# Optimization experiments

Hardware: AMD Instinct MI355X
Metric: run time of the kernel (lower is better)

The kernel has to match this reference:

```python
import jax, jax.numpy as jnp
import numpy as np

B, S, E = 2, 2048, 1024
H, D = 16, 64
BASE = 10000.0


def rotate_half(x):
    x1, x2 = jnp.split(x, 2, axis=-1)
    return jnp.concatenate((-x2, x1), axis=-1)


def rope_cos_sin(seq_len, dim):
    inv_freq = 1.0 / (BASE ** (jnp.arange(0, dim, 2, dtype=jnp.float32) / dim))
    t = jnp.arange(seq_len, dtype=jnp.float32)
    freqs = jnp.einsum('i,j->ij', t, inv_freq)          # [S, D/2]
    emb = jnp.concatenate((freqs, freqs), axis=-1)       # [S, D]
    return jnp.cos(emb), jnp.sin(emb)


def setup_inputs() -> dict:
    key = jax.random.key(0)
    ks = jax.random.split(key, 9)
    s = 1.0 / np.sqrt(E)
    inp = {
        'x': jax.random.normal(ks[0], (B, S, E), dtype=jnp.float32),
        'mask': jnp.ones((B, S), dtype=jnp.int32),
        'Wq': jax.random.normal(ks[1], (E, H * D), dtype=jnp.float32) * s,
        'bq': jnp.zeros((H * D,), dtype=jnp.float32),
        'Wk': jax.random.normal(ks[2], (E, H * D), dtype=jnp.float32) * s,
        'bk': jnp.zeros((H * D,), dtype=jnp.float32),
        'Wv': jax.random.normal(ks[3], (E, H * D), dtype=jnp.float32) * s,
        'bv': jnp.zeros((H * D,), dtype=jnp.float32),
        'Wo': jax.random.normal(ks[4], (H * D, E), dtype=jnp.float32) * s,
        'bo': jnp.zeros((E,), dtype=jnp.float32),
    }
    return inp


def reference(x, mask, Wq, bq, Wk, bk, Wv, bv, Wo, bo):
    b, s, _ = x.shape
    scale = D ** (-0.5)
    # projections -> [B, H, S, D]
    q = (x @ Wq + bq).reshape(b, s, H, D).transpose(0, 2, 1, 3)
    k = (x @ Wk + bk).reshape(b, s, H, D).transpose(0, 2, 1, 3)
    v = (x @ Wv + bv).reshape(b, s, H, D).transpose(0, 2, 1, 3)
    # rotary position embedding
    cos, sin = rope_cos_sin(s, D)                      # [S, D]
    cos = cos[None, None]
    sin = sin[None, None]
    q = q * cos + rotate_half(q) * sin
    k = k * cos + rotate_half(k) * sin
    # scores [B, H, S, S]
    scores = jnp.einsum('bhqd,bhkd->bhqk', q, k) * scale
    # padding mask [B,1,1,S]
    scores = jnp.where(mask[:, None, None, :] == 0, -jnp.inf, scores)
    # causal mask
    i = jnp.arange(s)
    causal = jnp.where(i[None, :] > i[:, None], -jnp.inf, 0.0)  # [S, S]
    scores = scores + causal[None, None]
    attn = jax.nn.softmax(scores, axis=-1)
    ctx = jnp.einsum('bhqk,bhkd->bhqd', attn, v)
    ctx = ctx.transpose(0, 2, 1, 3).reshape(b, s, H * D)
    return ctx @ Wo + bo
```

## Files before the change

kernel.cpp:

```cpp
#include <hip/hip_runtime.h>
#include <cstdint>
#include <cstddef>

#define DEVI __device__ __forceinline__

typedef __bf16 bf16_t;
typedef __bf16 bf16x4 __attribute__((ext_vector_type(4)));
typedef __bf16 bf16x8 __attribute__((ext_vector_type(8)));
typedef float  f32x4  __attribute__((ext_vector_type(4)));
typedef unsigned short u16x4 __attribute__((ext_vector_type(4)));

static constexpr int Bz = 2, S = 2048, E = 1024, H = 16, Dh = 64;
static constexpr int M  = Bz * S;
static constexpr int N  = H * Dh;
static constexpr int Kd = E;

DEVI unsigned short f2bf(float f) {
  unsigned u = __builtin_bit_cast(unsigned, f);
  return (unsigned short)((u + 0x7fffu + ((u >> 16) & 1u)) >> 16);
}

DEVI void async_copy16(void* lds, const void* g) {
  __builtin_amdgcn_global_load_lds((__attribute__((address_space(1))) void*)(g),
                                   (__attribute__((address_space(3))) void*)(lds), 16, 0, 0);
}

__global__ void prep_kernel(const float* __restrict__ x, bf16_t* __restrict__ xb,
                            const float* __restrict__ Wq, const float* __restrict__ Wk,
                            const float* __restrict__ Wv, const float* __restrict__ Wo,
                            bf16_t* __restrict__ WtBase,
                            float* __restrict__ ropeC, float* __restrict__ ropeS) {
  __shared__ unsigned short tile[64][68];
  const int blk = blockIdx.x, tid = threadIdx.x;
  if (blk < 4096) {
    int i = blk * 256 + tid;
    float4 v = ((const float4*)x)[i];
    u16x4 o = { f2bf(v.x), f2bf(v.y), f2bf(v.z), f2bf(v.w) };
    ((u16x4*)xb)[i] = o;
  } else if (blk < 5120) {
    const int i = blk - 4096;
    const int z = i >> 8, rest = i & 255;
    const int n0 = (rest & 15) * 64, k0 = (rest >> 4) * 64;
    const float* W = (z == 0) ? Wq : (z == 1) ? Wk : (z == 2) ? Wv : Wo;
    unsigned short* T = (unsigned short*)(WtBase + (size_t)z * Kd * N);
    for (int e = tid; e < 1024; e += 256) {
      int r = e >> 4, c4 = (e & 15) * 4;
      float4 v = *(const float4*)(W + (size_t)(k0 + r) * N + n0 + c4);
      u16x4 o = { f2bf(v.x), f2bf(v.y), f2bf(v.z), f2bf(v.w) };
      *(u16x4*)&tile[r][c4] = o;
    }
    __syncthreads();
    for (int e = tid; e < 1024; e += 256) {
      int r = e >> 4, c4 = (e & 15) * 4;
      u16x4 o = { tile[c4][r], tile[c4 + 1][r], tile[c4 + 2][r], tile[c4 + 3][r] };
      *(u16x4*)&T[(size_t)(n0 + r) * Kd + k0 + c4] = o;
    }
  } else {
    int i = (blk - 5120) * 256 + tid;
    int pos = i >> 5, j = i & 31;
    float inv = exp2f(-(float)j * 0.41524101186092029f);
    float ang = (float)pos * inv;
    ropeC[i] = cosf(ang);
    ropeS[i] = sinf(ang);
  }
}

__global__ void vtrans_kernel(const bf16_t* __restrict__ V, bf16_t* __restrict__ Vt) {
  __shared__ unsigned short tile[64][68];
  const int bh = blockIdx.y;
  const int s0 = blockIdx.x * 64;
  const unsigned short* Vp = (const unsigned short*)V + (size_t)bh * S * Dh;
  unsigned short* Tp = (unsigned short*)Vt + (size_t)bh * Dh * S;
  const int tid = threadIdx.x;
  for (int e = tid; e < 1024; e += 256) {
    int r = e >> 4, c4 = (e & 15) * 4;
    u16x4 v = *(const u16x4*)(Vp + (size_t)(s0 + r) * Dh + c4);
    *(u16x4*)&tile[r][c4] = v;
  }
  __syncthreads();
  for (int e = tid; e < 1024; e += 256) {
    int d = e >> 4, s4 = (e & 15) * 4;
    u16x4 o = { tile[s4][d], tile[s4 + 1][d], tile[s4 + 2][d], tile[s4 + 3][d] };
    *(u16x4*)&Tp[(size_t)d * S + s0 + s4] = o;
  }
}


DEVI void gemm_mainloop(const bf16_t* __restrict__ A, const bf16_t* __restrict__ Bt,
                        bf16_t* sA, bf16_t* sB, int m0, int n0, f32x4 (&acc)[4][4]) {
  const int tid  = threadIdx.x;
  const int lane = tid & 63;
  const int wid  = tid >> 6;
  const int l16  = lane & 15;
  const int quad = lane >> 4;
  const int wm = (wid >> 1) * 64;
  const int wn = (wid & 1) * 64;
  const int o0 = wid * 2048 + lane * 16;
  const int o1 = o0 + 1024;
  const int r0 = o0 >> 6, c0 = o0 & 63;
  const int r1 = o1 >> 6, c1 = o1 & 63;
  const char* Ab = (const char*)A;
  const char* Bb = (const char*)Bt;
  char* sAc = (char*)sA;
  char* sBc = (char*)sB;

  for (int k0 = 0; k0 < Kd; k0 += 32) {
    __syncthreads();
    async_copy16(sAc + wid * 2048,        Ab + ((size_t)(m0 + r0) * Kd + k0) * 2 + c0);
    async_copy16(sAc + wid * 2048 + 1024, Ab + ((size_t)(m0 + r1) * Kd + k0) * 2 + c1);
    async_copy16(sBc + wid * 2048,        Bb + ((size_t)(n0 + r0) * Kd + k0) * 2 + c0);
    async_copy16(sBc + wid * 2048 + 1024, Bb + ((size_t)(n0 + r1) * Kd + k0) * 2 + c1);
    __syncthreads();
    bf16x8 af[4], bfv[4];
#pragma unroll
    for (int mi = 0; mi < 4; ++mi)
      af[mi] = *(const bf16x8*)(sA + (wm + mi * 16 + l16) * 32 + quad * 8);
#pragma unroll
    for (int ni = 0; ni < 4; ++ni)
      bfv[ni] = *(const bf16x8*)(sB + (wn + ni * 16 + l16) * 32 + quad * 8);
#pragma unroll
    for (int mi = 0; mi < 4; ++mi)
#pragma unroll
      for (int ni = 0; ni < 4; ++ni)
        acc[mi][ni] = __builtin_amdgcn_mfma_f32_16x16x32_bf16(af[mi], bfv[ni], acc[mi][ni], 0, 0, 0);
  }
}

__global__ __launch_bounds__(256, 3) void gemm_qkv_kernel(
    const bf16_t* __restrict__ xb, const bf16_t* __restrict__ WtBase,
    const float* __restrict__ bq, const float* __restrict__ bk, const float* __restrict__ bv,
    bf16_t* __restrict__ outBase,
    const float* __restrict__ ropeC, const float* __restrict__ ropeS) {
  __shared__ bf16_t sA[4096], sB[4096];
  const int z = blockIdx.z;
  const bf16_t* Bt = WtBase + (size_t)z * Kd * N;
  const float* bias = (z == 0) ? bq : (z == 1) ? bk : bv;
  unsigned short* outp = (unsigned short*)(outBase + (size_t)z * M * N);
  const int n0 = blockIdx.x * 128, m0 = blockIdx.y * 128;
  f32x4 acc[4][4] = {};
  gemm_mainloop(xb, Bt, sA, sB, m0, n0, acc);

  const int tid = threadIdx.x, lane = tid & 63, wid = tid >> 6;
  const int l16 = lane & 15, quad = lane >> 4;
  const int wm = (wid >> 1) * 64, wn = (wid & 1) * 64;
  const int cbase = n0 + wn;
  const int h = cbase >> 6;

  if (z < 2) {
    const float qs = (z == 0) ? 0.18033688011112042f : 1.0f;
#pragma unroll
    for (int mi = 0; mi < 4; ++mi)
#pragma unroll
      for (int r = 0; r < 4; ++r) {
        int t = m0 + wm + mi * 16 + quad * 4 + r;
        int bb = t >> 11, s = t & (S - 1);
        size_t obase = ((size_t)(bb * H + h) * S + s) * Dh;
#pragma unroll
        for (int np = 0; np < 2; ++np) {
          int j = np * 16 + l16;
          float cc = ropeC[s * 32 + j];
          float ss = ropeS[s * 32 + j];
          float xlo = acc[mi][np][r]     + bias[cbase + j];
          float xhi = acc[mi][np + 2][r] + bias[cbase + j + 32];
          outp[obase + j]      = f2bf((xlo * cc - xhi * ss) * qs);
          outp[obase + j + 32] = f2bf((xhi * cc + xlo * ss) * qs);
        }
      }
  } else {
#pragma unroll
    for (int mi = 0; mi < 4; ++mi)
#pragma unroll
      for (int r = 0; r < 4; ++r) {
        int t = m0 + wm + mi * 16 + quad * 4 + r;
        int bb = t >> 11, s = t & (S - 1);
        size_t obase = ((size_t)(bb * H + h) * S + s) * Dh;
#pragma unroll
        for (int ni = 0; ni < 4; ++ni) {
          int d = ni * 16 + l16;
          outp[obase + d] = f2bf(acc[mi][ni][r] + bias[cbase + d]);
        }
      }
  }
}

__global__ __launch_bounds__(256, 4) void gemm_o_kernel(
    const bf16_t* __restrict__ A, const bf16_t* __restrict__ Bt,
    const float* __restrict__ bias, float* __restrict__ out) {
  __shared__ bf16_t sA[2048], sB[4096];
  const int n0 = blockIdx.x * 128, m0 = blockIdx.y * 64;
  const int tid = threadIdx.x, lane = tid & 63, wid = tid >> 6;
  const int l16 = lane & 15, quad = lane >> 4;
  const int wm = (wid >> 1) * 32, wn = (wid & 1) * 64;
  const int rowoff = lane >> 2, col8 = (lane & 3) * 8;
  const char* Ab = (const char*)A;
  const char* Bb = (const char*)Bt;
  char* sAc = (char*)sA;
  char* sBc = (char*)sB;
  f32x4 acc[2][4] = {};

  for (int k0 = 0; k0 < Kd; k0 += 32) {
    __syncthreads();
    async_copy16(sAc + wid * 1024,
                 Ab + ((size_t)(m0 + wid * 16 + rowoff) * Kd + k0 + col8) * 2);
    async_copy16(sBc + (wid * 2) * 1024,
                 Bb + ((size_t)(n0 + wid * 32 + rowoff) * Kd + k0 + col8) * 2);
    async_copy16(sBc + (wid * 2 + 1) * 1024,
                 Bb + ((size_t)(n0 + wid * 32 + 16 + rowoff) * Kd + k0 + col8) * 2);
    __syncthreads();
    bf16x8 af[2], bfv[4];
#pragma unroll
    for (int mi = 0; mi < 2; ++mi)
      af[mi] = *(const bf16x8*)(sA + (wm + mi * 16 + l16) * 32 + quad * 8);
#pragma unroll
    for (int ni = 0; ni < 4; ++ni)
      bfv[ni] = *(const bf16x8*)(sB + (wn + ni * 16 + l16) * 32 + quad * 8);
#pragma unroll
    for (int mi = 0; mi < 2; ++mi)
#pragma unroll
      for (int ni = 0; ni < 4; ++ni)
        acc[mi][ni] = __builtin_amdgcn_mfma_f32_16x16x32_bf16(af[mi], bfv[ni], acc[mi][ni], 0, 0, 0);
  }
#pragma unroll
  for (int mi = 0; mi < 2; ++mi)
#pragma unroll
    for (int r = 0; r < 4; ++r) {
      int t = m0 + wm + mi * 16 + quad * 4 + r;
#pragma unroll
      for (int ni = 0; ni < 4; ++ni) {
        int c = n0 + wn + ni * 16 + l16;
        out[(size_t)t * N + c] = acc[mi][ni][r] + bias[c];
      }
    }
}

__global__ __launch_bounds__(256, 3) void attn_kernel(
    const bf16_t* __restrict__ Q, const bf16_t* __restrict__ Kb,
    const bf16_t* __restrict__ Vt, const int* __restrict__ mask,
    bf16_t* __restrict__ ctx) {
  __shared__ bf16_t sK[8192];
  __shared__ bf16_t sV[8192];
  __shared__ unsigned short sP[4][16 * 136];

  const int tid = threadIdx.x, lane = tid & 63, wid = tid >> 6;
  const int l16 = lane & 15, quad = lane >> 4;

  const int idx = blockIdx.x;
  const int qb  = 31 - (idx >> 5);
  const int bh  = idx & 31;
  const int b   = bh >> 4;
  const int q0  = qb * 64;
  const int qw  = q0 + wid * 16;

  const bf16_t* Qp = Q + ((size_t)bh * S + qw) * Dh;
  const char*   Kg = (const char*)(Kb + (size_t)bh * S * Dh);
  const char*   Vg = (const char*)(Vt + (size_t)bh * Dh * S);
  const int*    mp = mask + b * S;

  bf16x8 qf0 = *(const bf16x8*)(Qp + l16 * Dh + quad * 8);
  bf16x8 qf1 = *(const bf16x8*)(Qp + l16 * Dh + 32 + quad * 8);

  int    sLds[4];
  size_t kGo[4], vGo[4];
#pragma unroll
  for (int i = 0; i < 4; ++i) {
    int sk = wid * 4 + i;
    int g = sk >> 1, c = sk & 1;
    sLds[i] = sk * 1024;
    kGo[i] = ((size_t)(g * 16 + l16) * Dh + c * 32 + quad * 8) * 2;
    vGo[i] = ((size_t)(wid * 16 + l16) * S + i * 32 + quad * 8) * 2;
  }
  char* sKc = (char*)sK;
  char* sVc = (char*)sV;

  f32x4 acc[4] = {};
  float lsum = 0.f;
  const int qcol = qw + l16;
  const int niter = (qb >> 1) + 1;
  unsigned short* pb = &sP[wid][0];

  for (int kt = 0; kt < niter; ++kt) {
    const int kb = kt * 128;
    __syncthreads();
#pragma unroll
    for (int i = 0; i < 4; ++i) {
      async_copy16(sKc + sLds[i], Kg + (size_t)kb * (Dh * 2) + kGo[i]);
      async_copy16(sVc + sLds[i], Vg + (size_t)kb * 2 + vGo[i]);
    }
    int mk0 = mp[kb + lane];
    int mk1 = mp[kb + 64 + lane];
    __syncthreads();

    f32x4 st[8];
#pragma unroll
    for (int g = 0; g < 8; ++g) {
      bf16x8 kf0 = *(const bf16x8*)(sK + (g * 2 + 0) * 512 + lane * 8);
      bf16x8 kf1 = *(const bf16x8*)(sK + (g * 2 + 1) * 512 + lane * 8);
      f32x4 z = {};
      z = __builtin_amdgcn_mfma_f32_16x16x32_bf16(kf0, qf0, z, 0, 0, 0);
      z = __builtin_amdgcn_mfma_f32_16x16x32_bf16(kf1, qf1, z, 0, 0, 0);
      st[g] = z;
    }

    unsigned long long dm0 = __ballot(mk0 == 0);
    unsigned long long dm1 = __ballot(mk1 == 0);
    if (dm0 | dm1) {
#pragma unroll
      for (int g = 0; g < 8; ++g) {
        unsigned long long dm = (g < 4) ? dm0 : dm1;
#pragma unroll
        for (int r = 0; r < 4; ++r)
          if ((dm >> ((g & 3) * 16 + quad * 4 + r)) & 1ull) st[g][r] = -1e30f;
      }
    }
    if (kt == niter - 1) {
#pragma unroll
      for (int g = 0; g < 8; ++g)
#pragma unroll
        for (int r = 0; r < 4; ++r)
          if (kb + g * 16 + quad * 4 + r > qcol) st[g][r] = -1e30f;
    }

#pragma unroll
    for (int g = 0; g < 8; ++g) {
      float e0 = exp2f(st[g][0]), e1 = exp2f(st[g][1]);
      float e2 = exp2f(st[g][2]), e3 = exp2f(st[g][3]);
      lsum += (e0 + e1) + (e2 + e3);
      bf16x4 pk = { (bf16_t)e0, (bf16_t)e1, (bf16_t)e2, (bf16_t)e3 };
      *(bf16x4*)&pb[l16 * 136 + g * 16 + quad * 4] = pk;
    }
    bf16x8 pf[4];
#pragma unroll
    for (int kc = 0; kc < 4; ++kc)
      pf[kc] = *(const bf16x8*)((const bf16_t*)(const void*)pb + l16 * 136 + kc * 32 + quad * 8);

#pragma unroll
    for (int dt = 0; dt < 4; ++dt)
#pragma unroll
      for (int kc = 0; kc < 4; ++kc) {
        bf16x8 vf = *(const bf16x8*)(sV + (dt * 4 + kc) * 512 + lane * 8);
        acc[dt] = __builtin_amdgcn_mfma_f32_16x16x32_bf16(vf, pf[kc], acc[dt], 0, 0, 0);
      }
  }

  lsum += __shfl_xor(lsum, 16);
  lsum += __shfl_xor(lsum, 32);
  float inv = 1.0f / lsum;
  unsigned short* cp = (unsigned short*)ctx;
  size_t trow = ((size_t)(b * S + qw + l16)) * N + (size_t)(bh & 15) * Dh;
#pragma unroll
  for (int dt = 0; dt < 4; ++dt) {
    u16x4 o = { f2bf(acc[dt][0] * inv), f2bf(acc[dt][1] * inv),
                f2bf(acc[dt][2] * inv), f2bf(acc[dt][3] * inv) };
    *(u16x4*)&cp[trow + dt * 16 + quad * 4] = o;
  }
}


extern "C" void kernel_launch(void* const* d_in, const int* in_sizes, int n_in,
                              void* d_out, int out_size, void* d_ws, size_t ws_size,
                              hipStream_t stream) {
  const float* x  = (const float*)d_in[0];
  const int*  msk = (const int*)d_in[1];
  const float* Wq = (const float*)d_in[2];
  const float* bq = (const float*)d_in[3];
  const float* Wk = (const float*)d_in[4];
  const float* bk = (const float*)d_in[5];
  const float* Wv = (const float*)d_in[6];
  const float* bv = (const float*)d_in[7];
  const float* Wo = (const float*)d_in[8];
  const float* bo = (const float*)d_in[9];
  float* out = (float*)d_out;
  (void)in_sizes; (void)n_in; (void)out_size; (void)ws_size;

  char* ws = (char*)d_ws;
  bf16_t* xb   = (bf16_t*)(ws);
  bf16_t* WT   = (bf16_t*)(ws + (8u  << 20));
  bf16_t* qkv  = (bf16_t*)(ws + (16u << 20));
  bf16_t* Qb   = qkv;
  bf16_t* Kbuf = qkv + (size_t)1 * M * N;
  bf16_t* Vb   = qkv + (size_t)2 * M * N;
  bf16_t* Vt   = xb;
  bf16_t* ctx  = Vb;
  float* ropeC = (float*)(ws + (40u << 20));
  float* ropeS = ropeC + (size_t)S * 32;

  prep_kernel<<<5376, 256, 0, stream>>>(x, xb, Wq, Wk, Wv, Wo, WT, ropeC, ropeS);
  gemm_qkv_kernel<<<dim3(8, 32, 3), 256, 0, stream>>>(xb, WT, bq, bk, bv, qkv, ropeC, ropeS);
  vtrans_kernel<<<dim3(32, 32), 256, 0, stream>>>(Vb, Vt);
  attn_kernel<<<1024, 256, 0, stream>>>(Qb, Kbuf, Vt, msk, ctx);
  gemm_o_kernel<<<dim3(8, 64), 256, 0, stream>>>(ctx, WT + (size_t)3 * Kd * N, bo, out);
}
```

Baseline: 197.9 us.

## Double-buffer GEMM and attention tiles; switch attention to 32x32 MFMA with 128-row query blocks

Both GEMM mainloops and the attention kernel now double-buffer their LDS tiles, issuing the async global-to-LDS copy for the next K step before computing on the current one, and drop one barrier per iteration. The attention kernel is restructured so each wave handles 32 query rows with 32x32x16 bf16 MFMAs over 64-key tiles, in 128-row query blocks with half as many workgroups. Waves skip key tiles that lie fully beyond their causal limit. The aim is to hide load latency and raise MFMA efficiency, at the cost of more LDS per block, possible occupancy loss and a new output-normalisation path through LDS.

```diff
diff --git a/kernel.cpp b/kernel.cpp
--- a/kernel.cpp
+++ b/kernel.cpp
@@ -8,6 +8,7 @@
 typedef __bf16 bf16x4 __attribute__((ext_vector_type(4)));
 typedef __bf16 bf16x8 __attribute__((ext_vector_type(8)));
 typedef float  f32x4  __attribute__((ext_vector_type(4)));
+typedef float  f32x16 __attribute__((ext_vector_type(16)));
 typedef unsigned short u16x4 __attribute__((ext_vector_type(4)));
 
 static constexpr int Bz = 2, S = 2048, E = 1024, H = 16, Dh = 64;
@@ -104,20 +105,26 @@
   char* sAc = (char*)sA;
   char* sBc = (char*)sB;
 
-  for (int k0 = 0; k0 < Kd; k0 += 32) {
+  auto stage = [&](int buf, int k0) {
+    async_copy16(sAc + buf * 8192 + wid * 2048,        Ab + ((size_t)(m0 + r0) * Kd + k0) * 2 + c0);
+    async_copy16(sAc + buf * 8192 + wid * 2048 + 1024, Ab + ((size_t)(m0 + r1) * Kd + k0) * 2 + c1);
+    async_copy16(sBc + buf * 8192 + wid * 2048,        Bb + ((size_t)(n0 + r0) * Kd + k0) * 2 + c0);
+    async_copy16(sBc + buf * 8192 + wid * 2048 + 1024, Bb + ((size_t)(n0 + r1) * Kd + k0) * 2 + c1);
+  };
+
+  stage(0, 0);
+  for (int i = 0; i < Kd / 32; ++i) {
     __syncthreads();
-    async_copy16(sAc + wid * 2048,        Ab + ((size_t)(m0 + r0) * Kd + k0) * 2 + c0);
-    async_copy16(sAc + wid * 2048 + 1024, Ab + ((size_t)(m0 + r1) * Kd + k0) * 2 + c1);
-    async_copy16(sBc + wid * 2048,        Bb + ((size_t)(n0 + r0) * Kd + k0) * 2 + c0);
-    async_copy16(sBc + wid * 2048 + 1024, Bb + ((size_t)(n0 + r1) * Kd + k0) * 2 + c1);
-    __syncthreads();
+    if (i + 1 < Kd / 32) stage((i + 1) & 1, (i + 1) * 32);
+    const bf16_t* a = sA + (i & 1) * 4096;
+    const bf16_t* b = sB + (i & 1) * 4096;
     bf16x8 af[4], bfv[4];
 #pragma unroll
     for (int mi = 0; mi < 4; ++mi)
-      af[mi] = *(const bf16x8*)(sA + (wm + mi * 16 + l16) * 32 + quad * 8);
+      af[mi] = *(const bf16x8*)(a + (wm + mi * 16 + l16) * 32 + quad * 8);
 #pragma unroll
     for (int ni = 0; ni < 4; ++ni)
-      bfv[ni] = *(const bf16x8*)(sB + (wn + ni * 16 + l16) * 32 + quad * 8);
+      bfv[ni] = *(const bf16x8*)(b + (wn + ni * 16 + l16) * 32 + quad * 8);
 #pragma unroll
     for (int mi = 0; mi < 4; ++mi)
 #pragma unroll
@@ -131,14 +138,14 @@
     const float* __restrict__ bq, const float* __restrict__ bk, const float* __restrict__ bv,
     bf16_t* __restrict__ outBase,
     const float* __restrict__ ropeC, const float* __restrict__ ropeS) {
-  __shared__ bf16_t sA[4096], sB[4096];
+  __shared__ bf16_t sA[2][4096], sB[2][4096];
   const int z = blockIdx.z;
   const bf16_t* Bt = WtBase + (size_t)z * Kd * N;
   const float* bias = (z == 0) ? bq : (z == 1) ? bk : bv;
   unsigned short* outp = (unsigned short*)(outBase + (size_t)z * M * N);
   const int n0 = blockIdx.x * 128, m0 = blockIdx.y * 128;
   f32x4 acc[4][4] = {};
-  gemm_mainloop(xb, Bt, sA, sB, m0, n0, acc);
+  gemm_mainloop(xb, Bt, &sA[0][0], &sB[0][0], m0, n0, acc);
 
   const int tid = threadIdx.x, lane = tid & 63, wid = tid >> 6;
   const int l16 = lane & 15, quad = lane >> 4;
@@ -186,7 +193,7 @@
 __global__ __launch_bounds__(256, 4) void gemm_o_kernel(
     const bf16_t* __restrict__ A, const bf16_t* __restrict__ Bt,
     const float* __restrict__ bias, float* __restrict__ out) {
-  __shared__ bf16_t sA[2048], sB[4096];
+  __shared__ bf16_t sA[2][2048], sB[2][4096];
   const int n0 = blockIdx.x * 128, m0 = blockIdx.y * 64;
   const int tid = threadIdx.x, lane = tid & 63, wid = tid >> 6;
   const int l16 = lane & 15, quad = lane >> 4;
@@ -198,22 +205,28 @@
   char* sBc = (char*)sB;
   f32x4 acc[2][4] = {};
 
-  for (int k0 = 0; k0 < Kd; k0 += 32) {
+  auto stage = [&](int buf, int k0) {
+    async_copy16(sAc + buf * 4096 + wid * 1024,
+                 Ab + ((size_t)(m0 + wid * 16 + rowoff) * Kd + k0 + col8) * 2);
+    async_copy16(sBc + buf * 8192 + (wid * 2) * 1024,
+                 Bb + ((size_t)(n0 + wid * 32 + rowoff) * Kd + k0 + col8) * 2);
+    async_copy16(sBc + buf * 8192 + (wid * 2 + 1) * 1024,
+                 Bb + ((size_t)(n0 + wid * 32 + 16 + rowoff) * Kd + k0 + col8) * 2);
+  };
+
+  stage(0, 0);
+  for (int i = 0; i < Kd / 32; ++i) {
     __syncthreads();
-    async_copy16(sAc + wid * 1024,
-                 Ab + ((size_t)(m0 + wid * 16 + rowoff) * Kd + k0 + col8) * 2);
-    async_copy16(sBc + (wid * 2) * 1024,
-                 Bb + ((size_t)(n0 + wid * 32 + rowoff) * Kd + k0 + col8) * 2);
-    async_copy16(sBc + (wid * 2 + 1) * 1024,
-                 Bb + ((size_t)(n0 + wid * 32 + 16 + rowoff) * Kd + k0 + col8) * 2);
-    __syncthreads();
+    if (i + 1 < Kd / 32) stage((i + 1) & 1, (i + 1) * 32);
+    const bf16_t* a = &sA[0][0] + (i & 1) * 2048;
+    const bf16_t* b = &sB[0][0] + (i & 1) * 4096;
     bf16x8 af[2], bfv[4];
 #pragma unroll
     for (int mi = 0; mi < 2; ++mi)
-      af[mi] = *(const bf16x8*)(sA + (wm + mi * 16 + l16) * 32 + quad * 8);
+      af[mi] = *(const bf16x8*)(a + (wm + mi * 16 + l16) * 32 + quad * 8);
 #pragma unroll
     for (int ni = 0; ni < 4; ++ni)
-      bfv[ni] = *(const bf16x8*)(sB + (wn + ni * 16 + l16) * 32 + quad * 8);
+      bfv[ni] = *(const bf16x8*)(b + (wn + ni * 16 + l16) * 32 + quad * 8);
 #pragma unroll
     for (int mi = 0; mi < 2; ++mi)
 #pragma unroll
@@ -237,122 +250,138 @@
     const bf16_t* __restrict__ Q, const bf16_t* __restrict__ Kb,
     const bf16_t* __restrict__ Vt, const int* __restrict__ mask,
     bf16_t* __restrict__ ctx) {
-  __shared__ bf16_t sK[8192];
-  __shared__ bf16_t sV[8192];
-  __shared__ unsigned short sP[4][16 * 136];
+  __shared__ bf16_t sK[2][4096];
+  __shared__ bf16_t sV[2][4096];
+  __shared__ unsigned short sP[4][32 * 72];
 
   const int tid = threadIdx.x, lane = tid & 63, wid = tid >> 6;
-  const int l16 = lane & 15, quad = lane >> 4;
-
-  const int idx = blockIdx.x;
-  const int qb  = 31 - (idx >> 5);
-  const int bh  = idx & 31;
-  const int b   = bh >> 4;
-  const int q0  = qb * 64;
-  const int qw  = q0 + wid * 16;
+  const int l32 = lane & 31, half = lane >> 5;
+
+  const int idx  = blockIdx.x;
+  const int qblk = 15 - (idx >> 5);
+  const int bh   = idx & 31;
+  const int b    = bh >> 4;
+  const int q0   = qblk * 128;
+  const int qw   = q0 + wid * 32;
 
   const bf16_t* Qp = Q + ((size_t)bh * S + qw) * Dh;
   const char*   Kg = (const char*)(Kb + (size_t)bh * S * Dh);
   const char*   Vg = (const char*)(Vt + (size_t)bh * Dh * S);
   const int*    mp = mask + b * S;
 
-  bf16x8 qf0 = *(const bf16x8*)(Qp + l16 * Dh + quad * 8);
-  bf16x8 qf1 = *(const bf16x8*)(Qp + l16 * Dh + 32 + quad * 8);
-
-  int    sLds[4];
-  size_t kGo[4], vGo[4];
-#pragma unroll
-  for (int i = 0; i < 4; ++i) {
-    int sk = wid * 4 + i;
-    int g = sk >> 1, c = sk & 1;
-    sLds[i] = sk * 1024;
-    kGo[i] = ((size_t)(g * 16 + l16) * Dh + c * 32 + quad * 8) * 2;
-    vGo[i] = ((size_t)(wid * 16 + l16) * S + i * 32 + quad * 8) * 2;
-  }
+  bf16x8 qf[4];
+#pragma unroll
+  for (int c = 0; c < 4; ++c)
+    qf[c] = *(const bf16x8*)(Qp + l32 * Dh + c * 16 + half * 8);
+
+  const int ks0 = wid * 2, ks1 = wid * 2 + 1;
+  const size_t kOff0 = (((size_t)((ks0 >> 2) * 32 + l32)) * Dh + (ks0 & 3) * 16 + half * 8) * 2;
+  const size_t kOff1 = (((size_t)((ks1 >> 2) * 32 + l32)) * Dh + (ks1 & 3) * 16 + half * 8) * 2;
+  const size_t vOff0 = (((size_t)((ks0 >> 2) * 32 + l32)) * S  + (ks0 & 3) * 16 + half * 8) * 2;
+  const size_t vOff1 = (((size_t)((ks1 >> 2) * 32 + l32)) * S  + (ks1 & 3) * 16 + half * 8) * 2;
   char* sKc = (char*)sK;
   char* sVc = (char*)sV;
 
-  f32x4 acc[4] = {};
+  auto stage = [&](int buf, int kt) {
+    size_t kbK = (size_t)kt * 64 * Dh * 2;
+    size_t kbV = (size_t)kt * 64 * 2;
+    async_copy16(sKc + buf * 8192 + ks0 * 1024, Kg + kbK + kOff0);
+    async_copy16(sKc + buf * 8192 + ks1 * 1024, Kg + kbK + kOff1);
+    async_copy16(sVc + buf * 8192 + ks0 * 1024, Vg + kbV + vOff0);
+    async_copy16(sVc + buf * 8192 + ks1 * 1024, Vg + kbV + vOff1);
+  };
+
+  f32x16 cacc[2] = {};
   float lsum = 0.f;
-  const int qcol = qw + l16;
-  const int niter = (qb >> 1) + 1;
+  const int qcol = qw + l32;
+  const int niter = 2 * (qblk + 1);
   unsigned short* pb = &sP[wid][0];
 
+  stage(0, 0);
   for (int kt = 0; kt < niter; ++kt) {
-    const int kb = kt * 128;
+    const int kb = kt * 64;
     __syncthreads();
-#pragma unroll
-    for (int i = 0; i < 4; ++i) {
-      async_copy16(sKc + sLds[i], Kg + (size_t)kb * (Dh * 2) + kGo[i]);
-      async_copy16(sVc + sLds[i], Vg + (size_t)kb * 2 + vGo[i]);
+    if (kt + 1 < niter) stage((kt + 1) & 1, kt + 1);
+    if (kb <= qw + 31) {
+      int mk = mp[kb + lane];
+      const bf16_t* kbuf = &sK[kt & 1][0];
+      const bf16_t* vbuf = &sV[kt & 1][0];
+
+      f32x16 st[2] = {};
+#pragma unroll
+      for (int g = 0; g < 2; ++g)
+#pragma unroll
+        for (int c = 0; c < 4; ++c) {
+          bf16x8 kf = *(const bf16x8*)(kbuf + (g * 4 + c) * 512 + lane * 8);
+          st[g] = __builtin_amdgcn_mfma_f32_32x32x16_bf16(kf, qf[c], st[g], 0, 0, 0);
+        }
+
+      unsigned long long dm = __ballot(mk == 0);
+      if (dm) {
+#pragma unroll
+        for (int g = 0; g < 2; ++g)
+#pragma unroll
+          for (int r = 0; r < 16; ++r) {
+            int krow = g * 32 + (r & 3) + 8 * (r >> 2) + 4 * half;
+            if ((dm >> krow) & 1ull) st[g][r] = -1e30f;
+          }
+      }
+      if (kb + 63 > qw) {
+#pragma unroll
+        for (int g = 0; g < 2; ++g)
+#pragma unroll
+          for (int r = 0; r < 16; ++r) {
+            int key = kb + g * 32 + (r & 3) + 8 * (r >> 2) + 4 * half;
+            if (key > qcol) st[g][r] = -1e30f;
+          }
+      }
+
+#pragma unroll
+      for (int g = 0; g < 2; ++g)
+#pragma unroll
+        for (int rg = 0; rg < 4; ++rg) {
+          float e0 = exp2f(st[g][rg * 4 + 0]);
+          float e1 = exp2f(st[g][rg * 4 + 1]);
+          float e2 = exp2f(st[g][rg * 4 + 2]);
+          float e3 = exp2f(st[g][rg * 4 + 3]);
+          lsum += (e0 + e1) + (e2 + e3);
+          bf16x4 pk = { (bf16_t)e0, (bf16_t)e1, (bf16_t)e2, (bf16_t)e3 };
+          *(bf16x4*)&pb[l32 * 72 + g * 32 + rg * 8 + half * 4] = pk;
+        }
+
+      bf16x8 pf[4];
+#pragma unroll
+      for (int c = 0; c < 4; ++c)
+        pf[c] = *(const bf16x8*)((const bf16_t*)(const void*)pb + l32 * 72 + c * 16 + half * 8);
+
+#pragma unroll
+      for (int dg = 0; dg < 2; ++dg)
+#pragma unroll
+        for (int c = 0; c < 4; ++c) {
+          bf16x8 vf = *(const bf16x8*)(vbuf + (dg * 4 + c) * 512 + lane * 8);
+          cacc[dg] = __builtin_amdgcn_mfma_f32_32x32x16_bf16(pf[c], vf, cacc[dg], 0, 0, 0);
+        }
     }
-    int mk0 = mp[kb + lane];
-    int mk1 = mp[kb + 64 + lane];
-    __syncthreads();
-
-    f32x4 st[8];
-#pragma unroll
-    for (int g = 0; g < 8; ++g) {
-      bf16x8 kf0 = *(const bf16x8*)(sK + (g * 2 + 0) * 512 + lane * 8);
-      bf16x8 kf1 = *(const bf16x8*)(sK + (g * 2 + 1) * 512 + lane * 8);
-      f32x4 z = {};
-      z = __builtin_amdgcn_mfma_f32_16x16x32_bf16(kf0, qf0, z, 0, 0, 0);
-      z = __builtin_amdgcn_mfma_f32_16x16x32_bf16(kf1, qf1, z, 0, 0, 0);
-      st[g] = z;
+  }
+
+  lsum += __shfl_xor(lsum, 32);
+  float iv = 1.0f / lsum;
+  float* ib = (float*)(void*)pb;
+  if (half == 0) ib[l32] = iv;
+  f32x4 ivq[4];
+#pragma unroll
+  for (int rg = 0; rg < 4; ++rg)
+    ivq[rg] = *(const f32x4*)&ib[rg * 8 + half * 4];
+
+  unsigned short* cp = (unsigned short*)ctx;
+  const size_t base = ((size_t)(b * S + qw)) * N + (size_t)(bh & 15) * 64;
+#pragma unroll
+  for (int dg = 0; dg < 2; ++dg)
+#pragma unroll
+    for (int r = 0; r < 16; ++r) {
+      int row = (r & 3) + 8 * (r >> 2) + 4 * half;
+      cp[base + (size_t)row * N + dg * 32 + l32] = f2bf(cacc[dg][r] * ivq[r >> 2][r & 3]);
     }
-
-    unsigned long long dm0 = __ballot(mk0 == 0);
-    unsigned long long dm1 = __ballot(mk1 == 0);
-    if (dm0 | dm1) {
-#pragma unroll
-      for (int g = 0; g < 8; ++g) {
-        unsigned long long dm = (g < 4) ? dm0 : dm1;
-#pragma unroll
-        for (int r = 0; r < 4; ++r)
-          if ((dm >> ((g & 3) * 16 + quad * 4 + r)) & 1ull) st[g][r] = -1e30f;
-      }
-    }
-    if (kt == niter - 1) {
-#pragma unroll
-      for (int g = 0; g < 8; ++g)
-#pragma unroll
-        for (int r = 0; r < 4; ++r)
-          if (kb + g * 16 + quad * 4 + r > qcol) st[g][r] = -1e30f;
-    }
-
-#pragma unroll
-    for (int g = 0; g < 8; ++g) {
-      float e0 = exp2f(st[g][0]), e1 = exp2f(st[g][1]);
-      float e2 = exp2f(st[g][2]), e3 = exp2f(st[g][3]);
-      lsum += (e0 + e1) + (e2 + e3);
-      bf16x4 pk = { (bf16_t)e0, (bf16_t)e1, (bf16_t)e2, (bf16_t)e3 };
-      *(bf16x4*)&pb[l16 * 136 + g * 16 + quad * 4] = pk;
-    }
-    bf16x8 pf[4];
-#pragma unroll
-    for (int kc = 0; kc < 4; ++kc)
-      pf[kc] = *(const bf16x8*)((const bf16_t*)(const void*)pb + l16 * 136 + kc * 32 + quad * 8);
-
-#pragma unroll
-    for (int dt = 0; dt < 4; ++dt)
-#pragma unroll
-      for (int kc = 0; kc < 4; ++kc) {
-        bf16x8 vf = *(const bf16x8*)(sV + (dt * 4 + kc) * 512 + lane * 8);
-        acc[dt] = __builtin_amdgcn_mfma_f32_16x16x32_bf16(vf, pf[kc], acc[dt], 0, 0, 0);
-      }
-  }
-
-  lsum += __shfl_xor(lsum, 16);
-  lsum += __shfl_xor(lsum, 32);
-  float inv = 1.0f / lsum;
-  unsigned short* cp = (unsigned short*)ctx;
-  size_t trow = ((size_t)(b * S + qw + l16)) * N + (size_t)(bh & 15) * Dh;
-#pragma unroll
-  for (int dt = 0; dt < 4; ++dt) {
-    u16x4 o = { f2bf(acc[dt][0] * inv), f2bf(acc[dt][1] * inv),
-                f2bf(acc[dt][2] * inv), f2bf(acc[dt][3] * inv) };
-    *(u16x4*)&cp[trow + dt * 16 + quad * 4] = o;
-  }
 }
 
 
@@ -387,6 +416,6 @@
   prep_kernel<<<5376, 256, 0, stream>>>(x, xb, Wq, Wk, Wv, Wo, WT, ropeC, ropeS);
   gemm_qkv_kernel<<<dim3(8, 32, 3), 256, 0, stream>>>(xb, WT, bq, bk, bv, qkv, ropeC, ropeS);
   vtrans_kernel<<<dim3(32, 32), 256, 0, stream>>>(Vb, Vt);
-  attn_kernel<<<1024, 256, 0, stream>>>(Qb, Kbuf, Vt, msk, ctx);
+  attn_kernel<<<512, 256, 0, stream>>>(Qb, Kbuf, Vt, msk, ctx);
   gemm_o_kernel<<<dim3(8, 64), 256, 0, stream>>>(ctx, WT + (size_t)3 * Kd * N, bo, out);
 }
```

Result: slower. 216.2 us (+9.2%).

## Fuse V transpose into QKV GEMM epilogue and double-buffer attention K/V tiles

Applied to the files above, without the earlier changes.

The V projection epilogue now transposes its tile through shared memory and writes V directly in [B,H,D,S] layout, so the separate vtrans kernel and its extra round trip through global memory go away. The attention kernel switches from 128-key single-buffered tiles to 64-key tiles with double-buffered async K/V loads. The next tile's load is issued before the current one is computed, so loads overlap with MFMA work. In exchange it runs twice as many loop iterations with smaller tiles, adds extra barriers in the QKV epilogue, and moves the workspace buffers to new offsets.

```diff
diff --git a/kernel.cpp b/kernel.cpp
--- a/kernel.cpp
+++ b/kernel.cpp
@@ -65,26 +65,6 @@
   }
 }
 
-__global__ void vtrans_kernel(const bf16_t* __restrict__ V, bf16_t* __restrict__ Vt) {
-  __shared__ unsigned short tile[64][68];
-  const int bh = blockIdx.y;
-  const int s0 = blockIdx.x * 64;
-  const unsigned short* Vp = (const unsigned short*)V + (size_t)bh * S * Dh;
-  unsigned short* Tp = (unsigned short*)Vt + (size_t)bh * Dh * S;
-  const int tid = threadIdx.x;
-  for (int e = tid; e < 1024; e += 256) {
-    int r = e >> 4, c4 = (e & 15) * 4;
-    u16x4 v = *(const u16x4*)(Vp + (size_t)(s0 + r) * Dh + c4);
-    *(u16x4*)&tile[r][c4] = v;
-  }
-  __syncthreads();
-  for (int e = tid; e < 1024; e += 256) {
-    int d = e >> 4, s4 = (e & 15) * 4;
-    u16x4 o = { tile[s4][d], tile[s4 + 1][d], tile[s4 + 2][d], tile[s4 + 3][d] };
-    *(u16x4*)&Tp[(size_t)d * S + s0 + s4] = o;
-  }
-}
-
 
 DEVI void gemm_mainloop(const bf16_t* __restrict__ A, const bf16_t* __restrict__ Bt,
                         bf16_t* sA, bf16_t* sB, int m0, int n0, f32x4 (&acc)[4][4]) {
@@ -129,16 +109,15 @@
 __global__ __launch_bounds__(256, 3) void gemm_qkv_kernel(
     const bf16_t* __restrict__ xb, const bf16_t* __restrict__ WtBase,
     const float* __restrict__ bq, const float* __restrict__ bk, const float* __restrict__ bv,
-    bf16_t* __restrict__ outBase,
+    bf16_t* __restrict__ outBase, bf16_t* __restrict__ Vt,
     const float* __restrict__ ropeC, const float* __restrict__ ropeS) {
-  __shared__ bf16_t sA[4096], sB[4096];
+  __shared__ bf16_t sM[8192];
   const int z = blockIdx.z;
   const bf16_t* Bt = WtBase + (size_t)z * Kd * N;
   const float* bias = (z == 0) ? bq : (z == 1) ? bk : bv;
-  unsigned short* outp = (unsigned short*)(outBase + (size_t)z * M * N);
   const int n0 = blockIdx.x * 128, m0 = blockIdx.y * 128;
   f32x4 acc[4][4] = {};
-  gemm_mainloop(xb, Bt, sA, sB, m0, n0, acc);
+  gemm_mainloop(xb, Bt, sM, sM + 4096, m0, n0, acc);
 
   const int tid = threadIdx.x, lane = tid & 63, wid = tid >> 6;
   const int l16 = lane & 15, quad = lane >> 4;
@@ -147,6 +126,7 @@
   const int h = cbase >> 6;
 
   if (z < 2) {
+    unsigned short* outp = (unsigned short*)(outBase + (size_t)z * M * N);
     const float qs = (z == 0) ? 0.18033688011112042f : 1.0f;
 #pragma unroll
     for (int mi = 0; mi < 4; ++mi)
@@ -167,17 +147,35 @@
         }
       }
   } else {
-#pragma unroll
-    for (int mi = 0; mi < 4; ++mi)
-#pragma unroll
-      for (int r = 0; r < 4; ++r) {
-        int t = m0 + wm + mi * 16 + quad * 4 + r;
-        int bb = t >> 11, s = t & (S - 1);
-        size_t obase = ((size_t)(bb * H + h) * S + s) * Dh;
-#pragma unroll
-        for (int ni = 0; ni < 4; ++ni) {
-          int d = ni * 16 + l16;
-          outp[obase + d] = f2bf(acc[mi][ni][r] + bias[cbase + d]);
+    const int bb = m0 >> 11, s0 = m0 & (S - 1);
+    const int head0 = n0 >> 6;
+    const int myh = wid & 1;
+    for (int hh = 0; hh < 2; ++hh)
+      for (int dq = 0; dq < 2; ++dq) {
+        __syncthreads();
+        if (myh == hh) {
+#pragma unroll
+          for (int ni2 = 0; ni2 < 2; ++ni2) {
+            int ni = dq * 2 + ni2;
+            int dloc = ni2 * 16 + l16;
+            float bv_ = bias[cbase + ni * 16 + l16];
+#pragma unroll
+            for (int mi = 0; mi < 4; ++mi)
+#pragma unroll
+              for (int r = 0; r < 4; ++r) {
+                int tloc = wm + mi * 16 + quad * 4 + r;
+                sM[dloc * 136 + tloc] = (bf16_t)(acc[mi][ni][r] + bv_);
+              }
+          }
+        }
+        __syncthreads();
+#pragma unroll
+        for (int rep = 0; rep < 2; ++rep) {
+          int cidx = rep * 256 + tid;
+          int dloc = cidx >> 4, chunk = cidx & 15;
+          bf16x8 v = *(const bf16x8*)&sM[dloc * 136 + chunk * 8];
+          size_t off = ((size_t)(bb * H + head0 + hh) * Dh + dq * 32 + dloc) * S + s0 + chunk * 8;
+          *(bf16x8*)(Vt + off) = v;
         }
       }
   }
@@ -237,9 +235,9 @@
     const bf16_t* __restrict__ Q, const bf16_t* __restrict__ Kb,
     const bf16_t* __restrict__ Vt, const int* __restrict__ mask,
     bf16_t* __restrict__ ctx) {
-  __shared__ bf16_t sK[8192];
-  __shared__ bf16_t sV[8192];
-  __shared__ unsigned short sP[4][16 * 136];
+  __shared__ bf16_t sK[2][4096];
+  __shared__ bf16_t sV[2][4096];
+  __shared__ unsigned short sP[4][16 * 72];
 
   const int tid = threadIdx.x, lane = tid & 63, wid = tid >> 6;
   const int l16 = lane & 15, quad = lane >> 4;
@@ -259,87 +257,82 @@
   bf16x8 qf0 = *(const bf16x8*)(Qp + l16 * Dh + quad * 8);
   bf16x8 qf1 = *(const bf16x8*)(Qp + l16 * Dh + 32 + quad * 8);
 
-  int    sLds[4];
-  size_t kGo[4], vGo[4];
-#pragma unroll
-  for (int i = 0; i < 4; ++i) {
-    int sk = wid * 4 + i;
-    int g = sk >> 1, c = sk & 1;
-    sLds[i] = sk * 1024;
-    kGo[i] = ((size_t)(g * 16 + l16) * Dh + c * 32 + quad * 8) * 2;
-    vGo[i] = ((size_t)(wid * 16 + l16) * S + i * 32 + quad * 8) * 2;
-  }
+  const size_t kOff0 = ((size_t)(wid * 16 + l16) * Dh + quad * 8) * 2;
+  const size_t kOff1 = kOff0 + 64;
+  const size_t vOff0 = ((size_t)(wid * 16 + l16) * S + quad * 8) * 2;
+  const size_t vOff1 = vOff0 + 64;
   char* sKc = (char*)sK;
   char* sVc = (char*)sV;
+
+  auto stage = [&](int buf, int kt) {
+    size_t kbK = (size_t)kt * 64 * Dh * 2;
+    size_t kbV = (size_t)kt * 64 * 2;
+    async_copy16(sKc + buf * 8192 + wid * 2048,        Kg + kbK + kOff0);
+    async_copy16(sKc + buf * 8192 + wid * 2048 + 1024, Kg + kbK + kOff1);
+    async_copy16(sVc + buf * 8192 + wid * 2048,        Vg + kbV + vOff0);
+    async_copy16(sVc + buf * 8192 + wid * 2048 + 1024, Vg + kbV + vOff1);
+  };
 
   f32x4 acc[4] = {};
   float lsum = 0.f;
   const int qcol = qw + l16;
-  const int niter = (qb >> 1) + 1;
+  const int niter = qb + 1;
   unsigned short* pb = &sP[wid][0];
 
+  stage(0, 0);
   for (int kt = 0; kt < niter; ++kt) {
-    const int kb = kt * 128;
-    __syncthreads();
-#pragma unroll
-    for (int i = 0; i < 4; ++i) {
-      async_copy16(sKc + sLds[i], Kg + (size_t)kb * (Dh * 2) + kGo[i]);
-      async_copy16(sVc + sLds[i], Vg + (size_t)kb * 2 + vGo[i]);
-    }
-    int mk0 = mp[kb + lane];
-    int mk1 = mp[kb + 64 + lane];
-    __syncthreads();
-
-    f32x4 st[8];
-#pragma unroll
-    for (int g = 0; g < 8; ++g) {
-      bf16x8 kf0 = *(const bf16x8*)(sK + (g * 2 + 0) * 512 + lane * 8);
-      bf16x8 kf1 = *(const bf16x8*)(sK + (g * 2 + 1) * 512 + lane * 8);
+    const int kb = kt * 64;
+    __syncthreads();
+    int mk = mp[kb + lane];
+    if (kt + 1 < niter) stage((kt + 1) & 1, kt + 1);
+    const bf16_t* kbuf = &sK[kt & 1][0];
+    const bf16_t* vbuf = &sV[kt & 1][0];
+
+    f32x4 st[4];
+#pragma unroll
+    for (int g = 0; g < 4; ++g) {
+      bf16x8 kf0 = *(const bf16x8*)(kbuf + (g * 2 + 0) * 512 + lane * 8);
+      bf16x8 kf1 = *(const bf16x8*)(kbuf + (g * 2 + 1) * 512 + lane * 8);
       f32x4 z = {};
       z = __builtin_amdgcn_mfma_f32_16x16x32_bf16(kf0, qf0, z, 0, 0, 0);
       z = __builtin_amdgcn_mfma_f32_16x16x32_bf16(kf1, qf1, z, 0, 0, 0);
       st[g] = z;
     }
 
-    unsigned long long dm0 = __ballot(mk0 == 0);
-    unsigned long long dm1 = __ballot(mk1 == 0);
-    if (dm0 | dm1) {
-#pragma unroll
-      for (int g = 0; g < 8; ++g) {
-        unsigned long long dm = (g < 4) ? dm0 : dm1;
+    unsigned long long dm = __ballot(mk == 0);
+    if (dm) {
+#pragma unroll
+      for (int g = 0; g < 4; ++g)
 #pragma unroll
         for (int r = 0; r < 4; ++r)
-          if ((dm >> ((g & 3) * 16 + quad * 4 + r)) & 1ull) st[g][r] = -1e30f;
-      }
+          if ((dm >> (g * 16 + quad * 4 + r)) & 1ull) st[g][r] = -1e30f;
     }
     if (kt == niter - 1) {
 #pragma unroll
-      for (int g = 0; g < 8; ++g)
+      for (int g = 0; g < 4; ++g)
 #pragma unroll
         for (int r = 0; r < 4; ++r)
           if (kb + g * 16 + quad * 4 + r > qcol) st[g][r] = -1e30f;
     }
 
 #pragma unroll
-    for (int g = 0; g < 8; ++g) {
+    for (int g = 0; g < 4; ++g) {
       float e0 = exp2f(st[g][0]), e1 = exp2f(st[g][1]);
       float e2 = exp2f(st[g][2]), e3 = exp2f(st[g][3]);
       lsum += (e0 + e1) + (e2 + e3);
       bf16x4 pk = { (bf16_t)e0, (bf16_t)e1, (bf16_t)e2, (bf16_t)e3 };
-      *(bf16x4*)&pb[l16 * 136 + g * 16 + quad * 4] = pk;
-    }
-    bf16x8 pf[4];
-#pragma unroll
-    for (int kc = 0; kc < 4; ++kc)
-      pf[kc] = *(const bf16x8*)((const bf16_t*)(const void*)pb + l16 * 136 + kc * 32 + quad * 8);
-
-#pragma unroll
-    for (int dt = 0; dt < 4; ++dt)
-#pragma unroll
-      for (int kc = 0; kc < 4; ++kc) {
-        bf16x8 vf = *(const bf16x8*)(sV + (dt * 4 + kc) * 512 + lane * 8);
-        acc[dt] = __builtin_amdgcn_mfma_f32_16x16x32_bf16(vf, pf[kc], acc[dt], 0, 0, 0);
-      }
+      *(bf16x4*)&pb[l16 * 72 + g * 16 + quad * 4] = pk;
+    }
+    bf16x8 pf0 = *(const bf16x8*)((const bf16_t*)(const void*)pb + l16 * 72 + quad * 8);
+    bf16x8 pf1 = *(const bf16x8*)((const bf16_t*)(const void*)pb + l16 * 72 + 32 + quad * 8);
+
+#pragma unroll
+    for (int dt = 0; dt < 4; ++dt) {
+      bf16x8 vf0 = *(const bf16x8*)(vbuf + (dt * 2 + 0) * 512 + lane * 8);
+      bf16x8 vf1 = *(const bf16x8*)(vbuf + (dt * 2 + 1) * 512 + lane * 8);
+      acc[dt] = __builtin_amdgcn_mfma_f32_16x16x32_bf16(vf0, pf0, acc[dt], 0, 0, 0);
+      acc[dt] = __builtin_amdgcn_mfma_f32_16x16x32_bf16(vf1, pf1, acc[dt], 0, 0, 0);
+    }
   }
 
   lsum += __shfl_xor(lsum, 16);
@@ -375,18 +368,15 @@
   char* ws = (char*)d_ws;
   bf16_t* xb   = (bf16_t*)(ws);
   bf16_t* WT   = (bf16_t*)(ws + (8u  << 20));
-  bf16_t* qkv  = (bf16_t*)(ws + (16u << 20));
-  bf16_t* Qb   = qkv;
-  bf16_t* Kbuf = qkv + (size_t)1 * M * N;
-  bf16_t* Vb   = qkv + (size_t)2 * M * N;
-  bf16_t* Vt   = xb;
-  bf16_t* ctx  = Vb;
+  bf16_t* Qb   = (bf16_t*)(ws + (16u << 20));
+  bf16_t* Kbuf = (bf16_t*)(ws + (24u << 20));
+  bf16_t* Vt   = (bf16_t*)(ws + (32u << 20));
   float* ropeC = (float*)(ws + (40u << 20));
   float* ropeS = ropeC + (size_t)S * 32;
+  bf16_t* ctx  = (bf16_t*)(ws + (41u << 20));
 
   prep_kernel<<<5376, 256, 0, stream>>>(x, xb, Wq, Wk, Wv, Wo, WT, ropeC, ropeS);
-  gemm_qkv_kernel<<<dim3(8, 32, 3), 256, 0, stream>>>(xb, WT, bq, bk, bv, qkv, ropeC, ropeS);
-  vtrans_kernel<<<dim3(32, 32), 256, 0, stream>>>(Vb, Vt);
+  gemm_qkv_kernel<<<dim3(8, 32, 3), 256, 0, stream>>>(xb, WT, bq, bk, bv, Qb, Vt, ropeC, ropeS);
   attn_kernel<<<1024, 256, 0, stream>>>(Qb, Kbuf, Vt, msk, ctx);
   gemm_o_kernel<<<dim3(8, 64), 256, 0, stream>>>(ctx, WT + (size_t)3 * Kd * N, bo, out);
 }
```

New measurement: 204.9 us. 3.5% more time.
